# Kernel tuning notes

Measured on AMD Instinct MI355X. Metric: run time of the kernel, lower is better.

Reference implementation:

```python
import jax, jax.numpy as jnp
import numpy as np

B, NQ, NK, C = 16, 8, 4096, 256
H = W = 64
HEADS = 8
CI = 128          # embedding_dim // attention_downsample_rate
HD = CI // HEADS  # per-head dim
EPS = float(np.finfo(np.float32).tiny)


def _gumbel_topk(scores, noise, n):
    # iterative gumbel-softmax top-k relaxation with straight-through hard k-hot
    g = scores + noise
    khot = jnp.zeros_like(g)
    onehot = jnp.zeros_like(g)
    for _ in range(n):
        g = g + jnp.log(jnp.maximum(1.0 - onehot, EPS))
        onehot = jax.nn.softmax(g, axis=-1)
        khot = khot + onehot
    _, ind = jax.lax.top_k(khot, n)
    rows = jnp.arange(khot.shape[0])[:, None]
    hard = jnp.zeros_like(khot).at[rows, ind].set(1.0)
    ret = hard - jax.lax.stop_gradient(khot) + khot  # == hard numerically
    return ret, jnp.sort(ind, axis=1)  # sorted idx = row-major order of boolean-mask select


def _sample_points(pe, content, ret, idx):
    # pe [H,W,C], content [b,H,W,C], ret [b,HW] k-hot, idx [b,k] sorted
    b = ret.shape[0]
    m = ret.reshape(b, H, W, 1)
    pe_m = (pe[None] * m).reshape(b, H * W, -1)
    c_m = (content * m).reshape(b, H * W, -1)
    take = lambda a: jnp.take_along_axis(a, idx[:, :, None], axis=1)
    return take(pe_m), take(c_m)


def _mlp(x, W1, b1, W2, b2, W3, b3):
    x = jax.nn.relu(x @ W1 + b1)
    x = jax.nn.relu(x @ W2 + b2)
    return x @ W3 + b3


def _forward(queries, keys, query_pe, key_pe, guiding_embedding, gumbel_p, gumbel_n,
             static_uncertain, static_refined, Wq, bq, Wk, bk, Wv, bv, Wo, bo,
             uW1, ub1, uW2, ub2, uW3, ub3, rW1, rb1, rW2, rb2, rW3, rb3,
             pe_gauss, point_pos, point_neg, n_sample_points):
    b = queries.shape[0]
    g = guiding_embedding.reshape(b, C, H * W).transpose(0, 2, 1)  # [b, HW, C]
    g = g * keys  # elementwise gating -> new guiding embedding

    # cross attention token -> image (internal dim CI, HEADS heads)
    def split_heads(x, Wx, bx):
        return (x @ Wx + bx).reshape(b, -1, HEADS, HD).transpose(0, 2, 1, 3)
    qh = split_heads(queries + query_pe, Wq, bq)
    kh = split_heads(g + key_pe, Wk, bk)
    vh = split_heads(g, Wv, bv)
    attn = jax.nn.softmax(jnp.einsum('bhqd,bhkd->bhqk', qh, kh) / np.float32(np.sqrt(HD)), axis=-1)
    out = jnp.einsum('bhqk,bhkd->bhqd', attn, vh).transpose(0, 2, 1, 3).reshape(b, -1, CI)
    queries = out @ Wo + bo  # [b, NQ, C]

    q1 = queries[:, 1, :]
    unc_tok = _mlp(jnp.concatenate([jnp.broadcast_to(static_uncertain, (b, C)), q1], -1),
                   uW1, ub1, uW2, ub2, uW3, ub3)
    ref_tok = _mlp(jnp.concatenate([jnp.broadcast_to(static_refined, (b, C)), q1], -1),
                   rW1, rb1, rW2, rb2, rW3, rb3)

    img = g.transpose(0, 2, 1)  # [b, C, HW]
    unc_norm = jax.nn.sigmoid(jnp.einsum('bc,bcn->bn', unc_tok, img))
    ref_mask = jnp.einsum('bc,bcn->bn', ref_tok, img)
    coarse_mask = jnp.einsum('bc,bcn->bn', q1, img)

    queries = jnp.concatenate([queries[:, 0:1], ref_tok[:, None, :], queries[:, 2:]], axis=1)

    # point-sampling reference map + gumbel-softmax top-k (training-path math)
    ref_map = unc_norm * (jax.nn.sigmoid(ref_mask) - jax.nn.sigmoid(coarse_mask))  # [b, HW]
    ret_p, idx_p = _gumbel_topk(ref_map, gumbel_p, n_sample_points)
    ret_n, idx_n = _gumbel_topk(-ref_map, gumbel_n, n_sample_points)

    # random fourier positional encoding of the 64x64 grid (SAM PositionEmbeddingRandom)
    xs = (jnp.arange(W, dtype=jnp.float32) + 0.5) / W
    ys = (jnp.arange(H, dtype=jnp.float32) + 0.5) / H
    coords = jnp.stack([jnp.tile(xs[None, :], (H, 1)), jnp.tile(ys[:, None], (1, W))], axis=-1)
    proj = ((2.0 * coords - 1.0) @ pe_gauss) * np.float32(2.0 * np.pi)  # [H, W, C//2]
    pe = jnp.concatenate([jnp.sin(proj), jnp.cos(proj)], axis=-1)       # [H, W, C]

    # F.interpolate of a 64x64 map to (64,64) is the identity here
    content = (keys + g).reshape(b, H, W, C)

    sp_pe, sp_c = _sample_points(pe, content, ret_p, idx_p)
    sn_pe, sn_c = _sample_points(pe, content, ret_n, idx_n)
    sp_pe = sp_pe + point_pos  # prompt_encoder.point_embeddings[1]
    sn_pe = sn_pe + point_neg  # prompt_encoder.point_embeddings[0]

    query_pe = jnp.concatenate([query_pe, sp_pe, sn_pe], axis=1)
    queries = jnp.concatenate([queries, sp_c, sn_c], axis=1)
    # pack (queries, query_pe) into one array for a single-output reference
    return jnp.concatenate([queries, query_pe], axis=1)  # [b, 2*(NQ+2k), C]


def setup_inputs():
    key = jax.random.key(0)
    ks = iter(jax.random.split(key, 48))
    n = lambda shape, s=1.0: jax.random.normal(next(ks), shape, jnp.float32) * s
    z = lambda shape: jnp.zeros(shape, jnp.float32)
    return {
        'queries': n((B, NQ, C)),
        'keys': n((B, NK, C)),
        'query_pe': n((B, NQ, C)),
        'key_pe': n((B, NK, C)),
        'guiding_embedding': n((B, C, H, W)),
        'gumbel_p': jax.random.gumbel(next(ks), (B, NK), jnp.float32),
        'gumbel_n': jax.random.gumbel(next(ks), (B, NK), jnp.float32),
        'static_uncertain': n((C,), 0.02),
        'static_refined': n((C,), 0.02),
        'Wq': n((C, CI), 0.02), 'bq': z((CI,)),
        'Wk': n((C, CI), 0.02), 'bk': z((CI,)),
        'Wv': n((C, CI), 0.02), 'bv': z((CI,)),
        'Wo': n((CI, C), 0.02), 'bo': z((C,)),
        'uW1': n((2 * C, C // 4), 0.05), 'ub1': z((C // 4,)),
        'uW2': n((C // 4, C // 4), 0.05), 'ub2': z((C // 4,)),
        'uW3': n((C // 4, C), 0.05), 'ub3': z((C,)),
        'rW1': n((2 * C, C // 4), 0.05), 'rb1': z((C // 4,)),
        'rW2': n((C // 4, C // 4), 0.05), 'rb2': z((C // 4,)),
        'rW3': n((C // 4, C), 0.05), 'rb3': z((C,)),
        'pe_gauss': n((2, C // 2)),
        'point_pos': n((C,), 0.02),
        'point_neg': n((C,), 0.02),
        'n_sample_points': 4,
    }


def reference(queries, keys, query_pe, key_pe, guiding_embedding, gumbel_p, gumbel_n,
              static_uncertain, static_refined, Wq, bq, Wk, bk, Wv, bv, Wo, bo,
              uW1, ub1, uW2, ub2, uW3, ub3, rW1, rb1, rW2, rb2, rW3, rb3,
              pe_gauss, point_pos, point_neg, n_sample_points):
    return _forward(queries, keys, query_pe, key_pe, guiding_embedding, gumbel_p, gumbel_n,
                    static_uncertain, static_refined, Wq, bq, Wk, bk, Wv, bv, Wo, bo,
                    uW1, ub1, uW2, ub2, uW3, ub3, rW1, rb1, rW2, rb2, rW3, rb3,
                    pe_gauss, point_pos, point_neg, n_sample_points)
```

## Files before the change

kernel.cpp:

```cpp
#include <hip/hip_runtime.h>

#define BB 16
#define NQn 8
#define NK 4096
#define CC 256
#define NHEADS 8
#define CIn 128
#define HDn 16
#define NHQ 64
#define EPS_TINY 1.17549435e-38f

constexpr size_t OFF_QK   = 0;
constexpr size_t OFF_QBK  = OFF_QK  + (size_t)BB*CC*NHQ;
constexpr size_t OFF_SC   = OFF_QBK + (size_t)BB*NHQ;
constexpr size_t OFF_MP   = OFF_SC  + (size_t)BB*NK*NHQ;
constexpr size_t OFF_SP   = OFF_MP  + (size_t)BB*32*NHQ;
constexpr size_t OFF_M    = OFF_SP  + (size_t)BB*32*NHQ;
constexpr size_t OFF_RS   = OFF_M   + (size_t)BB*NHQ;
constexpr size_t OFF_AVP  = OFF_RS  + (size_t)BB*NHQ;
constexpr size_t OFF_QATT = OFF_AVP + (size_t)BB*16*NHQ*CC;
constexpr size_t OFF_UNC  = OFF_QATT+ (size_t)BB*NQn*CC;
constexpr size_t OFF_REFT = OFF_UNC + (size_t)BB*CC;
constexpr size_t OFF_RMAP = OFF_REFT+ (size_t)BB*CC;
constexpr size_t OFF_IDX  = OFF_RMAP+ (size_t)BB*NK;
constexpr size_t OFF_RV   = OFF_IDX + 128;
constexpr size_t OFF_G    = OFF_RV  + 128;

__global__ __launch_bounds__(256) void k1_qside(
    const float* __restrict__ queries, const float* __restrict__ query_pe,
    const float* __restrict__ Wq, const float* __restrict__ bq,
    const float* __restrict__ Wk, const float* __restrict__ bk,
    float* __restrict__ ws)
{
  int b = blockIdx.x >> 3, q = blockIdx.x & 7, t = threadIdx.x;
  __shared__ float x[CC];
  __shared__ float qh[CIn];
  x[t] = queries[(b*NQn+q)*CC + t] + query_pe[(b*NQn+q)*CC + t];
  __syncthreads();
  if (t < CIn) {
    float a = bq[t];
    for (int c = 0; c < CC; ++c) a += x[c]*Wq[c*CIn + t];
    qh[t] = a * 0.25f;
  }
  __syncthreads();
  float* Qk = ws + OFF_QK;
  #pragma unroll
  for (int h = 0; h < NHEADS; ++h) {
    float a = 0.f;
    #pragma unroll
    for (int d = 0; d < HDn; ++d) a += qh[h*HDn+d] * Wk[t*CIn + h*HDn + d];
    Qk[((size_t)b*CC + t)*NHQ + h*NQn + q] = a;
  }
  if (t < NHEADS) {
    float a = 0.f;
    #pragma unroll
    for (int d = 0; d < HDn; ++d) a += qh[t*HDn+d] * bk[t*HDn+d];
    (ws + OFF_QBK)[b*NHQ + t*NQn + q] = a;
  }
}

__global__ __launch_bounds__(256, 8) void k2_scores(
    const float* __restrict__ keys, const float* __restrict__ key_pe,
    const float* __restrict__ guiding, float* __restrict__ ws)
{
  int b = blockIdx.y, n0 = blockIdx.x * 32, t = threadIdx.x;
  __shared__ __align__(16) float Xs[32][36];
  __shared__ __align__(16) float Qs[32][64];
  __shared__ float Gt[32][33];
  const float* Qk = ws + OFF_QK + (size_t)b*CC*NHQ;
  float* G = ws + OFF_G;
  const int tx = t & 15, ty = t >> 4;
  const int xr = t >> 3, xc4 = (t & 7) * 4;
  const int gn = t & 31, gc0 = (t >> 5) * 4;
  float acc[2][4] = {};

  float gld[4]; float4 kp, pp; float qp[8];
  {
    #pragma unroll
    for (int i = 0; i < 4; ++i)
      gld[i] = guiding[((size_t)b*CC + gc0 + i)*NK + n0 + gn];
    size_t kb = ((size_t)b*NK + n0 + xr)*CC + xc4;
    kp = *(const float4*)&keys[kb];
    pp = *(const float4*)&key_pe[kb];
    #pragma unroll
    for (int i = 0; i < 8; ++i) {
      int l = i*256 + t;
      qp[i] = Qk[(size_t)(l>>6)*NHQ + (l & 63)];
    }
  }
  for (int ch = 0; ch < 8; ++ch) {
    int c0 = ch*32;
    #pragma unroll
    for (int i = 0; i < 4; ++i) Gt[gc0 + i][gn] = gld[i];
    __syncthreads();
    #pragma unroll
    for (int i = 0; i < 8; ++i) {
      int l = i*256 + t;
      Qs[l>>6][l&63] = qp[i];
    }
    {
      size_t kbase = ((size_t)b*NK + n0 + xr)*CC + c0 + xc4;
      float4 g4;
      g4.x = kp.x * Gt[xc4+0][xr];
      g4.y = kp.y * Gt[xc4+1][xr];
      g4.z = kp.z * Gt[xc4+2][xr];
      g4.w = kp.w * Gt[xc4+3][xr];
      *(float4*)&G[kbase] = g4;
      float4 o; o.x=g4.x+pp.x; o.y=g4.y+pp.y; o.z=g4.z+pp.z; o.w=g4.w+pp.w;
      *(float4*)&Xs[xr][xc4] = o;
    }
    __syncthreads();
    if (ch < 7) {
      int c1 = c0 + 32;
      #pragma unroll
      for (int i = 0; i < 4; ++i)
        gld[i] = guiding[((size_t)b*CC + c1 + gc0 + i)*NK + n0 + gn];
      size_t kb2 = ((size_t)b*NK + n0 + xr)*CC + c1 + xc4;
      kp = *(const float4*)&keys[kb2];
      pp = *(const float4*)&key_pe[kb2];
      #pragma unroll
      for (int i = 0; i < 8; ++i) {
        int l = i*256 + t;
        qp[i] = Qk[(size_t)(c1 + (l>>6))*NHQ + (l & 63)];
      }
    }
    #pragma unroll
    for (int cb = 0; cb < 8; ++cb) {
      float4 x0 = *(const float4*)&Xs[2*ty][4*cb];
      float4 x1 = *(const float4*)&Xs[2*ty+1][4*cb];
      #pragma unroll
      for (int u = 0; u < 4; ++u) {
        float4 qf = *(const float4*)&Qs[4*cb+u][4*tx];
        float xu0 = ((const float*)&x0)[u];
        float xu1 = ((const float*)&x1)[u];
        acc[0][0] += xu0*qf.x; acc[0][1] += xu0*qf.y; acc[0][2] += xu0*qf.z; acc[0][3] += xu0*qf.w;
        acc[1][0] += xu1*qf.x; acc[1][1] += xu1*qf.y; acc[1][2] += xu1*qf.z; acc[1][3] += xu1*qf.w;
      }
    }
  }
  const float* qbk = ws + OFF_QBK + (size_t)b*NHQ;
  float qb[4] = {qbk[4*tx], qbk[4*tx+1], qbk[4*tx+2], qbk[4*tx+3]};
  float* sc = ws + OFF_SC + ((size_t)b*NK + n0)*NHQ;
  #pragma unroll
  for (int i = 0; i < 2; ++i) {
    float4 o;
    o.x = acc[i][0]+qb[0]; o.y = acc[i][1]+qb[1]; o.z = acc[i][2]+qb[2]; o.w = acc[i][3]+qb[3];
    *(float4*)&sc[(size_t)(2*ty + i)*NHQ + 4*tx] = o;
  }
}

__global__ __launch_bounds__(256) void k3a_stats(float* __restrict__ ws)
{
  int b = blockIdx.y, sb = blockIdx.x, t = threadIdx.x;
  int hq = t & 63, r = t >> 6;
  const float* sc = ws + OFF_SC + ((size_t)b*NK + sb*128)*NHQ;
  float m = -INFINITY, s = 0.f;
  for (int i = 0; i < 32; ++i) {
    float v = sc[(r + 4*i)*NHQ + hq];
    if (v > m) { s = s*expf(m - v) + 1.f; m = v; } else { s += expf(v - m); }
  }
  __shared__ float rm[256], rs[256];
  rm[t] = m; rs[t] = s;
  __syncthreads();
  if (t < 64) {
    float m0=rm[t], m1=rm[t+64], m2=rm[t+128], m3=rm[t+192];
    float mm = fmaxf(fmaxf(m0,m1), fmaxf(m2,m3));
    float ss = rs[t]*expf(m0-mm) + rs[t+64]*expf(m1-mm) + rs[t+128]*expf(m2-mm) + rs[t+192]*expf(m3-mm);
    (ws + OFF_MP)[(b*32 + sb)*NHQ + t] = mm;
    (ws + OFF_SP)[(b*32 + sb)*NHQ + t] = ss;
  }
}

__global__ __launch_bounds__(64) void k3b_combine(float* __restrict__ ws)
{
  int b = blockIdx.x, hq = threadIdx.x;
  const float* mp = ws + OFF_MP + (size_t)b*32*NHQ;
  const float* sp = ws + OFF_SP + (size_t)b*32*NHQ;
  float m = -INFINITY;
  #pragma unroll
  for (int i = 0; i < 32; ++i) m = fmaxf(m, mp[i*NHQ+hq]);
  float s = 0.f;
  #pragma unroll
  for (int i = 0; i < 32; ++i) s += sp[i*NHQ+hq]*expf(mp[i*NHQ+hq]-m);
  (ws+OFF_M)[b*NHQ+hq] = m;
  (ws+OFF_RS)[b*NHQ+hq] = 1.0f/s;
}

__global__ __launch_bounds__(256) void k4_av(float* __restrict__ ws)
{
  int kb = blockIdx.x, ch = blockIdx.y, b = blockIdx.z, t = threadIdx.x;
  int k0 = kb * 256, cbase = ch * 64;
  __shared__ __align__(16) float gld[32][68];
  __shared__ __align__(16) float wld[32][64];
  __shared__ float mv[64], rv[64];
  if (t < 64) { mv[t] = (ws+OFF_M)[b*NHQ+t]; rv[t] = (ws+OFF_RS)[b*NHQ+t]; }
  int hq0 = (t & 15) * 4, c0 = (t >> 4) * 4;
  int sr = t >> 4, sc4 = (t & 15) * 4;
  float accf[4][4] = {};
  const float* sc = ws + OFF_SC;
  const float* G  = ws + OFF_G;
  __syncthreads();
  for (int kk = 0; kk < 256; kk += 32) {
    #pragma unroll
    for (int p = 0; p < 2; ++p)
      *(float4*)&gld[p*16 + sr][sc4] =
        *(const float4*)&G[((size_t)b*NK + k0+kk + p*16 + sr)*CC + cbase + sc4];
    #pragma unroll
    for (int i = 0; i < 8; ++i) {
      int l = i*256 + t; int k = l >> 6, hq = l & 63;
      float v = sc[((size_t)b*NK + k0+kk+k)*NHQ + hq];
      wld[k][hq] = expf(v - mv[hq]) * rv[hq];
    }
    __syncthreads();
    #pragma unroll 4
    for (int k = 0; k < 32; ++k) {
      float4 w4 = *(const float4*)&wld[k][hq0];
      float4 gv = *(const float4*)&gld[k][c0];
      float wq[4] = {w4.x, w4.y, w4.z, w4.w};
      float gq[4] = {gv.x, gv.y, gv.z, gv.w};
      #pragma unroll
      for (int i = 0; i < 4; ++i)
        #pragma unroll
        for (int j = 0; j < 4; ++j) accf[i][j] += wq[i]*gq[j];
    }
    __syncthreads();
  }
  float* avp = ws + OFF_AVP + (((size_t)b*16 + kb)*NHQ)*CC;
  #pragma unroll
  for (int i = 0; i < 4; ++i) {
    float4 o;
    o.x = accf[i][0]; o.y = accf[i][1]; o.z = accf[i][2]; o.w = accf[i][3];
    *(float4*)&avp[(size_t)(hq0 + i)*CC + cbase + c0] = o;
  }
}

__global__ __launch_bounds__(256) void k56_attout(
    const float* __restrict__ Wv, const float* __restrict__ bv,
    const float* __restrict__ Wo, const float* __restrict__ bo,
    float* __restrict__ ws)
{
  int b = blockIdx.x >> 3, q = blockIdx.x & 7, t = threadIdx.x;
  __shared__ float avs[NHEADS][CC];
  __shared__ float outv[CIn];
  const float* avp = ws + OFF_AVP;
  #pragma unroll
  for (int h = 0; h < NHEADS; ++h) {
    int hq = h*NQn + q;
    float a = 0.f;
    #pragma unroll 4
    for (int kb = 0; kb < 16; ++kb)
      a += avp[(((size_t)b*16 + kb)*NHQ + hq)*CC + t];
    avs[h][t] = a;
  }
  __syncthreads();
  if (t < CIn) {
    int h = t >> 4;
    float a = bv[t];
    for (int c = 0; c < CC; ++c) a += avs[h][c]*Wv[c*CIn + t];
    outv[t] = a;
  }
  __syncthreads();
  float a = bo[t];
  for (int ci = 0; ci < CIn; ++ci) a += outv[ci]*Wo[ci*CC + t];
  (ws+OFF_QATT)[((size_t)b*NQn + q)*CC + t] = a;
}

__global__ __launch_bounds__(256) void k7_mlps(
    const float* __restrict__ su, const float* __restrict__ sr,
    const float* __restrict__ uW1, const float* __restrict__ ub1,
    const float* __restrict__ uW2, const float* __restrict__ ub2,
    const float* __restrict__ uW3, const float* __restrict__ ub3,
    const float* __restrict__ rW1, const float* __restrict__ rb1,
    const float* __restrict__ rW2, const float* __restrict__ rb2,
    const float* __restrict__ rW3, const float* __restrict__ rb3,
    float* __restrict__ ws)
{
  int b = blockIdx.x, t = threadIdx.x;
  __shared__ float xs[768];
  __shared__ float h1[2][64], h2[2][64];
  xs[t] = su[t];
  xs[256+t] = (ws+OFF_QATT)[((size_t)b*NQn + 1)*CC + t];
  xs[512+t] = sr[t];
  __syncthreads();
  if (t < 128) {
    int which = t >> 6, o = t & 63;
    const float* W1 = which ? rW1 : uW1;
    const float* b1 = which ? rb1 : ub1;
    int base = which ? 512 : 0;
    float a = b1[o];
    for (int i = 0; i < 256; ++i) a += xs[base+i]*W1[i*64 + o];
    for (int i = 0; i < 256; ++i) a += xs[256+i]*W1[(256+i)*64 + o];
    h1[which][o] = fmaxf(a, 0.f);
  }
  __syncthreads();
  if (t < 128) {
    int which = t >> 6, o = t & 63;
    const float* W2 = which ? rW2 : uW2;
    const float* b2 = which ? rb2 : ub2;
    float a = b2[o];
    #pragma unroll 8
    for (int i = 0; i < 64; ++i) a += h1[which][i]*W2[i*64+o];
    h2[which][o] = fmaxf(a, 0.f);
  }
  __syncthreads();
  {
    float a = ub3[t];
    #pragma unroll 8
    for (int i = 0; i < 64; ++i) a += h2[0][i]*uW3[i*CC + t];
    (ws+OFF_UNC)[b*CC + t] = a;
    float a2 = rb3[t];
    #pragma unroll 8
    for (int i = 0; i < 64; ++i) a2 += h2[1][i]*rW3[i*CC + t];
    (ws+OFF_REFT)[b*CC + t] = a2;
  }
}

__global__ __launch_bounds__(256) void k8_masks(float* __restrict__ ws)
{
  int b = blockIdx.y, t = threadIdx.x;
  int wave = t >> 6, lane = t & 63;
  __shared__ float q1s[CC], us[CC], rts[CC];
  q1s[t] = (ws+OFF_QATT)[((size_t)b*NQn+1)*CC + t];
  us[t]  = (ws+OFF_UNC)[b*CC + t];
  rts[t] = (ws+OFF_REFT)[b*CC + t];
  __syncthreads();
  float q1v[4], usv[4], rtv[4];
  #pragma unroll
  for (int u = 0; u < 4; ++u) {
    q1v[u] = q1s[lane*4+u]; usv[u] = us[lane*4+u]; rtv[u] = rts[lane*4+u];
  }
  const float* G = ws + OFF_G;
  float* rmap = ws + OFF_RMAP + (size_t)b*NK;
  int n_base = blockIdx.x*32 + wave*8;
  for (int r = 0; r < 8; ++r) {
    int n = n_base + r;
    float4 gv = *(const float4*)&G[((size_t)b*NK + n)*CC + lane*4];
    float aq = gv.x*q1v[0] + gv.y*q1v[1] + gv.z*q1v[2] + gv.w*q1v[3];
    float au = gv.x*usv[0] + gv.y*usv[1] + gv.z*usv[2] + gv.w*usv[3];
    float ar = gv.x*rtv[0] + gv.y*rtv[1] + gv.z*rtv[2] + gv.w*rtv[3];
    #pragma unroll
    for (int s = 1; s < 64; s <<= 1) {
      aq += __shfl_xor(aq, s, 64);
      au += __shfl_xor(au, s, 64);
      ar += __shfl_xor(ar, s, 64);
    }
    if (lane == 0) {
      float un = 1.f/(1.f+expf(-au));
      rmap[n] = un * (1.f/(1.f+expf(-ar)) - 1.f/(1.f+expf(-aq)));
    }
  }
}

__global__ __launch_bounds__(256) void k9_gumbel(
    const float* __restrict__ gp, const float* __restrict__ gn,
    float* __restrict__ ws)
{
  int sign = blockIdx.x, b = blockIdx.y, t = threadIdx.x;
  int wave = t >> 6, lane = t & 63;
  const float* noise = sign ? gn : gp;
  const float* rmap = ws + OFF_RMAP + (size_t)b*NK;
  float g[16], kh[16], oh[16];
  #pragma unroll
  for (int i = 0; i < 16; ++i) {
    int n = i*256 + t;
    float scv = rmap[n];
    if (sign) scv = -scv;
    g[i] = scv + noise[(size_t)b*NK + n];
    kh[i] = 0.f; oh[i] = 0.f;
  }
  __shared__ float wred[8];
  __shared__ float selV[16];
  __shared__ int   selIdx[16];
  for (int it = 0; it < 4; ++it) {
    if (it > 0) {
      #pragma unroll
      for (int i = 0; i < 16; ++i) g[i] += logf(fmaxf(1.f - oh[i], EPS_TINY));
    }
    float m = g[0];
    #pragma unroll
    for (int i = 1; i < 16; ++i) m = fmaxf(m, g[i]);
    #pragma unroll
    for (int s = 1; s < 64; s <<= 1) m = fmaxf(m, __shfl_xor(m, s, 64));
    if (lane == 0) wred[wave] = m;
    __syncthreads();
    m = fmaxf(fmaxf(wred[0], wred[1]), fmaxf(wred[2], wred[3]));
    float e[16], ls = 0.f;
    #pragma unroll
    for (int i = 0; i < 16; ++i) { e[i] = expf(g[i]-m); ls += e[i]; }
    #pragma unroll
    for (int s = 1; s < 64; s <<= 1) ls += __shfl_xor(ls, s, 64);
    if (lane == 0) wred[4+wave] = ls;
    __syncthreads();
    float ssum = wred[4]+wred[5]+wred[6]+wred[7];
    #pragma unroll
    for (int i = 0; i < 16; ++i) { oh[i] = e[i]/ssum; kh[i] += oh[i]; }
  }
  int id[4]; float rr[4];
  for (int j = 0; j < 4; ++j) {
    float bv = kh[0]; int bi = t;
    #pragma unroll
    for (int i = 1; i < 16; ++i) {
      if (kh[i] > bv) { bv = kh[i]; bi = i*256 + t; }
    }
    #pragma unroll
    for (int s = 1; s < 64; s <<= 1) {
      float ov = __shfl_xor(bv, s, 64);
      int   oi = __shfl_xor(bi, s, 64);
      if (ov > bv || (ov == bv && oi < bi)) { bv = ov; bi = oi; }
    }
    if (lane == 0) { selV[j*4+wave] = bv; selIdx[j*4+wave] = bi; }
    __syncthreads();
    bv = selV[j*4]; bi = selIdx[j*4];
    #pragma unroll
    for (int w = 1; w < 4; ++w) {
      float ov = selV[j*4+w]; int oi = selIdx[j*4+w];
      if (ov > bv || (ov == bv && oi < bi)) { bv = ov; bi = oi; }
    }
    id[j] = bi; rr[j] = (1.f - bv) + bv;
    if ((bi & 255) == t) kh[bi >> 8] = -1.f;
  }
  if (t == 0) {
    for (int a = 0; a < 3; ++a)
      for (int c2 = a+1; c2 < 4; ++c2)
        if (id[c2] < id[a]) { int ti=id[a]; id[a]=id[c2]; id[c2]=ti; float tr=rr[a]; rr[a]=rr[c2]; rr[c2]=tr; }
    int* iout = (int*)(ws + OFF_IDX);
    float* rout = ws + OFF_RV;
    for (int j = 0; j < 4; ++j) {
      iout[(sign*BB + b)*4 + j] = id[j];
      rout[(sign*BB + b)*4 + j] = rr[j];
    }
  }
}

__global__ __launch_bounds__(256) void k10_out(
    const float* __restrict__ keys, const float* __restrict__ query_pe,
    const float* __restrict__ point_pos, const float* __restrict__ point_neg,
    const float* __restrict__ pe_gauss,
    float* __restrict__ ws, float* __restrict__ out)
{
  int b = blockIdx.y, r = blockIdx.x, t = threadIdx.x;
  const float* G = ws + OFF_G;
  float val;
  if (r < 8) {
    val = (r == 1) ? (ws+OFF_REFT)[b*CC + t]
                   : (ws+OFF_QATT)[((size_t)b*NQn + r)*CC + t];
  } else if (r < 16) {
    int j = r - 8; int sign = j >> 2; int jj = j & 3;
    int idx = ((const int*)(ws+OFF_IDX))[(sign*BB + b)*4 + jj];
    float rvv = (ws+OFF_RV)[(sign*BB + b)*4 + jj];
    float kv = keys[((size_t)b*NK + idx)*CC + t];
    float gv = G[((size_t)b*NK + idx)*CC + t];
    val = (kv + gv) * rvv;
  } else if (r < 24) {
    val = query_pe[((size_t)b*NQn + (r-16))*CC + t];
  } else {
    int j = r - 24; int sign = j >> 2; int jj = j & 3;
    int idx = ((const int*)(ws+OFF_IDX))[(sign*BB + b)*4 + jj];
    float rvv = (ws+OFF_RV)[(sign*BB + b)*4 + jj];
    const float* point = sign ? point_neg : point_pos;
    int h = idx >> 6, w = idx & 63;
    float x = (w + 0.5f)/64.f, y = (h + 0.5f)/64.f;
    int jf = (t < 128) ? t : (t - 128);
    float proj = ((2.f*x - 1.f)*pe_gauss[jf] + (2.f*y - 1.f)*pe_gauss[128 + jf]) * 6.28318530717958647692f;
    float sv = (t < 128) ? sinf(proj) : cosf(proj);
    val = sv*rvv + point[t];
  }
  out[((size_t)b*32 + r)*CC + t] = val;
}

extern "C" void kernel_launch(void* const* d_in, const int* in_sizes, int n_in,
                              void* d_out, int out_size, void* d_ws, size_t ws_size,
                              hipStream_t stream)
{
  const float* queries   = (const float*)d_in[0];
  const float* keys      = (const float*)d_in[1];
  const float* query_pe  = (const float*)d_in[2];
  const float* key_pe    = (const float*)d_in[3];
  const float* guiding   = (const float*)d_in[4];
  const float* gumbel_p  = (const float*)d_in[5];
  const float* gumbel_n  = (const float*)d_in[6];
  const float* s_unc     = (const float*)d_in[7];
  const float* s_ref     = (const float*)d_in[8];
  const float* Wq  = (const float*)d_in[9];   const float* bq  = (const float*)d_in[10];
  const float* Wk  = (const float*)d_in[11];  const float* bk  = (const float*)d_in[12];
  const float* Wv  = (const float*)d_in[13];  const float* bv  = (const float*)d_in[14];
  const float* Wo  = (const float*)d_in[15];  const float* bo  = (const float*)d_in[16];
  const float* uW1 = (const float*)d_in[17];  const float* ub1 = (const float*)d_in[18];
  const float* uW2 = (const float*)d_in[19];  const float* ub2 = (const float*)d_in[20];
  const float* uW3 = (const float*)d_in[21];  const float* ub3 = (const float*)d_in[22];
  const float* rW1 = (const float*)d_in[23];  const float* rb1 = (const float*)d_in[24];
  const float* rW2 = (const float*)d_in[25];  const float* rb2 = (const float*)d_in[26];
  const float* rW3 = (const float*)d_in[27];  const float* rb3 = (const float*)d_in[28];
  const float* pe_gauss  = (const float*)d_in[29];
  const float* point_pos = (const float*)d_in[30];
  const float* point_neg = (const float*)d_in[31];
  float* ws = (float*)d_ws;
  float* out = (float*)d_out;

  k1_qside  <<<dim3(BB*NQn),    256, 0, stream>>>(queries, query_pe, Wq, bq, Wk, bk, ws);
  k2_scores <<<dim3(128, BB),   256, 0, stream>>>(keys, key_pe, guiding, ws);
  k3a_stats <<<dim3(32, BB),    256, 0, stream>>>(ws);
  k3b_combine<<<dim3(BB),        64, 0, stream>>>(ws);
  k4_av     <<<dim3(16, 4, BB), 256, 0, stream>>>(ws);
  k56_attout<<<dim3(BB*NQn),    256, 0, stream>>>(Wv, bv, Wo, bo, ws);
  k7_mlps   <<<dim3(BB),        256, 0, stream>>>(s_unc, s_ref, uW1, ub1, uW2, ub2, uW3, ub3,
                                                  rW1, rb1, rW2, rb2, rW3, rb3, ws);
  k8_masks  <<<dim3(128, BB),   256, 0, stream>>>(ws);
  k9_gumbel <<<dim3(2, BB),     256, 0, stream>>>(gumbel_p, gumbel_n, ws);
  k10_out   <<<dim3(32, BB),    256, 0, stream>>>(keys, query_pe, point_pos, point_neg,
                                                  pe_gauss, ws, out);
}
```

Measured before the change: 231.4 us.

## Fuse softmax partial stats into score kernel and enlarge key tile to 64

The score kernel now handles 64 keys per block instead of 32, with each thread computing a 4x4 register tile. It also computes per-block softmax max and sum-of-exp in shared memory, which removes the separate stats kernel and its re-read of the score buffer. The combine kernel reduces over 64 partials instead of 32. In exchange, the grid has half as many blocks, registers per thread rise, and the kernel does extra shared-memory reductions and barriers.

After: 211.7 us. 8.5% less time.

```diff
diff --git a/kernel.cpp b/kernel.cpp
--- a/kernel.cpp
+++ b/kernel.cpp
@@ -14,8 +14,8 @@
 constexpr size_t OFF_QBK  = OFF_QK  + (size_t)BB*CC*NHQ;
 constexpr size_t OFF_SC   = OFF_QBK + (size_t)BB*NHQ;
 constexpr size_t OFF_MP   = OFF_SC  + (size_t)BB*NK*NHQ;
-constexpr size_t OFF_SP   = OFF_MP  + (size_t)BB*32*NHQ;
-constexpr size_t OFF_M    = OFF_SP  + (size_t)BB*32*NHQ;
+constexpr size_t OFF_SP   = OFF_MP  + (size_t)BB*64*NHQ;
+constexpr size_t OFF_M    = OFF_SP  + (size_t)BB*64*NHQ;
 constexpr size_t OFF_RS   = OFF_M   + (size_t)BB*NHQ;
 constexpr size_t OFF_AVP  = OFF_RS  + (size_t)BB*NHQ;
 constexpr size_t OFF_QATT = OFF_AVP + (size_t)BB*16*NHQ*CC;
@@ -59,29 +59,30 @@
   }
 }
 
-__global__ __launch_bounds__(256, 8) void k2_scores(
+__global__ __launch_bounds__(256, 4) void k2_scores(
     const float* __restrict__ keys, const float* __restrict__ key_pe,
     const float* __restrict__ guiding, float* __restrict__ ws)
 {
-  int b = blockIdx.y, n0 = blockIdx.x * 32, t = threadIdx.x;
-  __shared__ __align__(16) float Xs[32][36];
+  int b = blockIdx.y, blk = blockIdx.x, n0 = blk * 64, t = threadIdx.x;
+  __shared__ __align__(16) float Xs[64][36];
   __shared__ __align__(16) float Qs[32][64];
-  __shared__ float Gt[32][33];
+  __shared__ float Gt[32][66];
   const float* Qk = ws + OFF_QK + (size_t)b*CC*NHQ;
   float* G = ws + OFF_G;
   const int tx = t & 15, ty = t >> 4;
-  const int xr = t >> 3, xc4 = (t & 7) * 4;
-  const int gn = t & 31, gc0 = (t >> 5) * 4;
-  float acc[2][4] = {};
-
-  float gld[4]; float4 kp, pp; float qp[8];
+  const int xr = t >> 2, xco = (t & 3) * 8;
+  const int gr = (t >> 6) * 8, gn = t & 63;
+  const int qc = t >> 3, qh = (t & 7) * 8;
+  float acc[4][4] = {};
+
+  float gld[8]; float4 k0v, k1v, p0v, p1v; float qp[8];
   {
     #pragma unroll
-    for (int i = 0; i < 4; ++i)
-      gld[i] = guiding[((size_t)b*CC + gc0 + i)*NK + n0 + gn];
-    size_t kb = ((size_t)b*NK + n0 + xr)*CC + xc4;
-    kp = *(const float4*)&keys[kb];
-    pp = *(const float4*)&key_pe[kb];
+    for (int i = 0; i < 8; ++i)
+      gld[i] = guiding[((size_t)b*CC + gr + i)*NK + n0 + gn];
+    size_t kb = ((size_t)b*NK + n0 + xr)*CC + xco;
+    k0v = *(const float4*)&keys[kb];   k1v = *(const float4*)&keys[kb+4];
+    p0v = *(const float4*)&key_pe[kb]; p1v = *(const float4*)&key_pe[kb+4];
     #pragma unroll
     for (int i = 0; i < 8; ++i) {
       int l = i*256 + t;
@@ -91,7 +92,7 @@
   for (int ch = 0; ch < 8; ++ch) {
     int c0 = ch*32;
     #pragma unroll
-    for (int i = 0; i < 4; ++i) Gt[gc0 + i][gn] = gld[i];
+    for (int i = 0; i < 8; ++i) Gt[gr + i][gn] = gld[i];
     __syncthreads();
     #pragma unroll
     for (int i = 0; i < 8; ++i) {
@@ -99,89 +100,105 @@
       Qs[l>>6][l&63] = qp[i];
     }
     {
-      size_t kbase = ((size_t)b*NK + n0 + xr)*CC + c0 + xc4;
-      float4 g4;
-      g4.x = kp.x * Gt[xc4+0][xr];
-      g4.y = kp.y * Gt[xc4+1][xr];
-      g4.z = kp.z * Gt[xc4+2][xr];
-      g4.w = kp.w * Gt[xc4+3][xr];
-      *(float4*)&G[kbase] = g4;
-      float4 o; o.x=g4.x+pp.x; o.y=g4.y+pp.y; o.z=g4.z+pp.z; o.w=g4.w+pp.w;
-      *(float4*)&Xs[xr][xc4] = o;
+      size_t kbase = ((size_t)b*NK + n0 + xr)*CC + c0 + xco;
+      float4 g0, g1;
+      g0.x = k0v.x * Gt[xco+0][xr]; g0.y = k0v.y * Gt[xco+1][xr];
+      g0.z = k0v.z * Gt[xco+2][xr]; g0.w = k0v.w * Gt[xco+3][xr];
+      g1.x = k1v.x * Gt[xco+4][xr]; g1.y = k1v.y * Gt[xco+5][xr];
+      g1.z = k1v.z * Gt[xco+6][xr]; g1.w = k1v.w * Gt[xco+7][xr];
+      *(float4*)&G[kbase]   = g0;
+      *(float4*)&G[kbase+4] = g1;
+      float4 x0, x1;
+      x0.x = g0.x+p0v.x; x0.y = g0.y+p0v.y; x0.z = g0.z+p0v.z; x0.w = g0.w+p0v.w;
+      x1.x = g1.x+p1v.x; x1.y = g1.y+p1v.y; x1.z = g1.z+p1v.z; x1.w = g1.w+p1v.w;
+      *(float4*)&Xs[xr][xco]   = x0;
+      *(float4*)&Xs[xr][xco+4] = x1;
     }
     __syncthreads();
     if (ch < 7) {
       int c1 = c0 + 32;
       #pragma unroll
-      for (int i = 0; i < 4; ++i)
-        gld[i] = guiding[((size_t)b*CC + c1 + gc0 + i)*NK + n0 + gn];
-      size_t kb2 = ((size_t)b*NK + n0 + xr)*CC + c1 + xc4;
-      kp = *(const float4*)&keys[kb2];
-      pp = *(const float4*)&key_pe[kb2];
+      for (int i = 0; i < 8; ++i)
+        gld[i] = guiding[((size_t)b*CC + c1 + gr + i)*NK + n0 + gn];
+      size_t kb2 = ((size_t)b*NK + n0 + xr)*CC + c1 + xco;
+      k0v = *(const float4*)&keys[kb2];   k1v = *(const float4*)&keys[kb2+4];
+      p0v = *(const float4*)&key_pe[kb2]; p1v = *(const float4*)&key_pe[kb2+4];
       #pragma unroll
       for (int i = 0; i < 8; ++i) {
         int l = i*256 + t;
         qp[i] = Qk[(size_t)(c1 + (l>>6))*NHQ + (l & 63)];
       }
     }
-    #pragma unroll
+    #pragma unroll 4
     for (int cb = 0; cb < 8; ++cb) {
-      float4 x0 = *(const float4*)&Xs[2*ty][4*cb];
-      float4 x1 = *(const float4*)&Xs[2*ty+1][4*cb];
+      float4 xf[4];
+      #pragma unroll
+      for (int i = 0; i < 4; ++i) xf[i] = *(const float4*)&Xs[4*ty+i][4*cb];
       #pragma unroll
       for (int u = 0; u < 4; ++u) {
         float4 qf = *(const float4*)&Qs[4*cb+u][4*tx];
-        float xu0 = ((const float*)&x0)[u];
-        float xu1 = ((const float*)&x1)[u];
-        acc[0][0] += xu0*qf.x; acc[0][1] += xu0*qf.y; acc[0][2] += xu0*qf.z; acc[0][3] += xu0*qf.w;
-        acc[1][0] += xu1*qf.x; acc[1][1] += xu1*qf.y; acc[1][2] += xu1*qf.z; acc[1][3] += xu1*qf.w;
+        float xu[4] = { ((const float*)&xf[0])[u], ((const float*)&xf[1])[u],
+                        ((const float*)&xf[2])[u], ((const float*)&xf[3])[u] };
+        #pragma unroll
+        for (int i = 0; i < 4; ++i) {
+          acc[i][0] += xu[i]*qf.x; acc[i][1] += xu[i]*qf.y;
+          acc[i][2] += xu[i]*qf.z; acc[i][3] += xu[i]*qf.w;
+        }
       }
     }
   }
   const float* qbk = ws + OFF_QBK + (size_t)b*NHQ;
   float qb[4] = {qbk[4*tx], qbk[4*tx+1], qbk[4*tx+2], qbk[4*tx+3]};
-  float* sc = ws + OFF_SC + ((size_t)b*NK + n0)*NHQ;
-  #pragma unroll
-  for (int i = 0; i < 2; ++i) {
-    float4 o;
-    o.x = acc[i][0]+qb[0]; o.y = acc[i][1]+qb[1]; o.z = acc[i][2]+qb[2]; o.w = acc[i][3]+qb[3];
-    *(float4*)&sc[(size_t)(2*ty + i)*NHQ + 4*tx] = o;
-  }
-}
-
-__global__ __launch_bounds__(256) void k3a_stats(float* __restrict__ ws)
-{
-  int b = blockIdx.y, sb = blockIdx.x, t = threadIdx.x;
-  int hq = t & 63, r = t >> 6;
-  const float* sc = ws + OFF_SC + ((size_t)b*NK + sb*128)*NHQ;
-  float m = -INFINITY, s = 0.f;
-  for (int i = 0; i < 32; ++i) {
-    float v = sc[(r + 4*i)*NHQ + hq];
-    if (v > m) { s = s*expf(m - v) + 1.f; m = v; } else { s += expf(v - m); }
-  }
-  __shared__ float rm[256], rs[256];
-  rm[t] = m; rs[t] = s;
+  float* scp = ws + OFF_SC + ((size_t)b*NK + n0)*NHQ;
+  #pragma unroll
+  for (int i = 0; i < 4; ++i) {
+    acc[i][0] += qb[0]; acc[i][1] += qb[1]; acc[i][2] += qb[2]; acc[i][3] += qb[3];
+    float4 o; o.x = acc[i][0]; o.y = acc[i][1]; o.z = acc[i][2]; o.w = acc[i][3];
+    *(float4*)&scp[(size_t)(4*ty + i)*NHQ + 4*tx] = o;
+  }
+  __syncthreads();
+  float* red  = &Qs[0][0];
+  float* mfin = &Gt[0][0];
+  #pragma unroll
+  for (int j = 0; j < 4; ++j) {
+    float lm = fmaxf(fmaxf(acc[0][j], acc[1][j]), fmaxf(acc[2][j], acc[3][j]));
+    red[ty*64 + 4*tx + j] = lm;
+  }
   __syncthreads();
   if (t < 64) {
-    float m0=rm[t], m1=rm[t+64], m2=rm[t+128], m3=rm[t+192];
-    float mm = fmaxf(fmaxf(m0,m1), fmaxf(m2,m3));
-    float ss = rs[t]*expf(m0-mm) + rs[t+64]*expf(m1-mm) + rs[t+128]*expf(m2-mm) + rs[t+192]*expf(m3-mm);
-    (ws + OFF_MP)[(b*32 + sb)*NHQ + t] = mm;
-    (ws + OFF_SP)[(b*32 + sb)*NHQ + t] = ss;
+    float m = red[t];
+    #pragma unroll
+    for (int r = 1; r < 16; ++r) m = fmaxf(m, red[r*64 + t]);
+    mfin[t] = m;
+  }
+  __syncthreads();
+  #pragma unroll
+  for (int j = 0; j < 4; ++j) {
+    float m = mfin[4*tx + j];
+    float ls = expf(acc[0][j]-m) + expf(acc[1][j]-m) + expf(acc[2][j]-m) + expf(acc[3][j]-m);
+    red[ty*64 + 4*tx + j] = ls;
+  }
+  __syncthreads();
+  if (t < 64) {
+    float s = 0.f;
+    #pragma unroll
+    for (int r = 0; r < 16; ++r) s += red[r*64 + t];
+    (ws + OFF_MP)[((size_t)b*64 + blk)*NHQ + t] = mfin[t];
+    (ws + OFF_SP)[((size_t)b*64 + blk)*NHQ + t] = s;
   }
 }
 
 __global__ __launch_bounds__(64) void k3b_combine(float* __restrict__ ws)
 {
   int b = blockIdx.x, hq = threadIdx.x;
-  const float* mp = ws + OFF_MP + (size_t)b*32*NHQ;
-  const float* sp = ws + OFF_SP + (size_t)b*32*NHQ;
+  const float* mp = ws + OFF_MP + (size_t)b*64*NHQ;
+  const float* sp = ws + OFF_SP + (size_t)b*64*NHQ;
   float m = -INFINITY;
-  #pragma unroll
-  for (int i = 0; i < 32; ++i) m = fmaxf(m, mp[i*NHQ+hq]);
+  #pragma unroll 8
+  for (int i = 0; i < 64; ++i) m = fmaxf(m, mp[i*NHQ+hq]);
   float s = 0.f;
-  #pragma unroll
-  for (int i = 0; i < 32; ++i) s += sp[i*NHQ+hq]*expf(mp[i*NHQ+hq]-m);
+  #pragma unroll 8
+  for (int i = 0; i < 64; ++i) s += sp[i*NHQ+hq]*expf(mp[i*NHQ+hq]-m);
   (ws+OFF_M)[b*NHQ+hq] = m;
   (ws+OFF_RS)[b*NHQ+hq] = 1.0f/s;
 }
@@ -498,8 +515,7 @@
   float* out = (float*)d_out;
 
   k1_qside  <<<dim3(BB*NQn),    256, 0, stream>>>(queries, query_pe, Wq, bq, Wk, bk, ws);
-  k2_scores <<<dim3(128, BB),   256, 0, stream>>>(keys, key_pe, guiding, ws);
-  k3a_stats <<<dim3(32, BB),    256, 0, stream>>>(ws);
+  k2_scores <<<dim3(64, BB),    256, 0, stream>>>(keys, key_pe, guiding, ws);
   k3b_combine<<<dim3(BB),        64, 0, stream>>>(ws);
   k4_av     <<<dim3(16, 4, BB), 256, 0, stream>>>(ws);
   k56_attout<<<dim3(BB*NQn),    256, 0, stream>>>(Wv, bv, Wo, bo, ws);
```
